# Kernel optimization log

Hardware: AMD Instinct MI355X
Metric: run time of the kernel (lower is better)

Reference implementation:

```python
import jax, jax.numpy as jnp
import numpy as np

N, E, R = 50000, 1600000, 8
IN_F, HID_F, OUT_F = 128, 64, 64


def setup_inputs() -> dict:
    key = jax.random.key(0)
    ks = jax.random.split(key, 9)
    x = jax.random.normal(ks[0], (N, IN_F), dtype=jnp.float32)
    edge_index = jax.random.randint(ks[1], (2, E), 0, N, dtype=jnp.int64)
    edge_type = jax.random.randint(ks[2], (E,), 0, R, dtype=jnp.int64)
    # layer 1 params (scaled like glorot)
    s1 = 1.0 / np.sqrt(IN_F)
    W1_rel = jax.random.normal(ks[3], (R, IN_F, HID_F), dtype=jnp.float32) * s1
    W1_root = jax.random.normal(ks[4], (IN_F, HID_F), dtype=jnp.float32) * s1
    b1 = jnp.zeros((HID_F,), dtype=jnp.float32)
    # layer 2 params
    s2 = 1.0 / np.sqrt(HID_F)
    W2_rel = jax.random.normal(ks[5], (R, HID_F, OUT_F), dtype=jnp.float32) * s2
    W2_root = jax.random.normal(ks[6], (HID_F, OUT_F), dtype=jnp.float32) * s2
    b2 = jnp.zeros((OUT_F,), dtype=jnp.float32)
    return {"x": x, "edge_index": edge_index, "edge_type": edge_type,
            "W1_rel": W1_rel, "W1_root": W1_root, "b1": b1,
            "W2_rel": W2_rel, "W2_root": W2_root, "b2": b2}


def _rgcn_conv(x, src, dst, etype, W_rel, W_root, b):
    """PyG RGCNConv: root transform + per-relation mean-aggregated messages."""
    n = x.shape[0]
    r = W_rel.shape[0]
    # per-relation transform of all node features: [R, N, H]
    xw = jnp.einsum('nd,rdh->rnh', x, W_rel)
    # per-edge message: transformed source feature under the edge's relation
    msg = xw[etype, src]  # [E, H]
    # mean normalization per (dst, relation) pair
    key = dst * r + etype  # [E]
    cnt = jax.ops.segment_sum(jnp.ones(etype.shape, dtype=x.dtype), key,
                              num_segments=n * r)
    inv = 1.0 / jnp.maximum(cnt, 1.0)
    msg = msg * inv[key][:, None]
    # scatter-add into target nodes
    agg = jax.ops.segment_sum(msg, dst, num_segments=n)  # [N, H]
    return agg + x @ W_root + b


def reference(x, edge_index, edge_type, W1_rel, W1_root, b1, W2_rel, W2_root, b2):
    src, dst = edge_index[0], edge_index[1]
    h = _rgcn_conv(x, src, dst, edge_type, W1_rel, W1_root, b1)
    h = jax.nn.relu(h)
    out = _rgcn_conv(h, src, dst, edge_type, W2_rel, W2_root, b2)
    return out
```

## Files before the change

kernel.cpp:

```cpp
#include <hip/hip_runtime.h>


constexpr int NN  = 50000;
constexpr int NE  = 1600000;
constexpr int NR  = 8;
constexpr int FIN = 128;
constexpr int FH  = 64;

constexpr int BSH = 7;
constexpr int BN  = 1 << BSH;
constexpr int NB  = (NN + BN - 1) >> BSH;
constexpr int CAP = 6144;
constexpr int CH  = 4096;
constexpr int NAPP = (NE + CH - 1) / CH;
constexpr unsigned XWMAX = (unsigned)(NN - 1) * (NR * 64) + (NR - 1) * 64;

typedef __attribute__((ext_vector_type(8))) short bf16x8;
typedef __attribute__((ext_vector_type(4))) short bf16x4;
typedef __attribute__((ext_vector_type(4))) float f32x4;

__device__ __forceinline__ unsigned short f2bf(float f) {
  unsigned u = __float_as_uint(f);
  u = (u + 0x7fff + ((u >> 16) & 1)) >> 16;
  return (unsigned short)u;
}
__device__ __forceinline__ float bf2f(unsigned short b) {
  return __uint_as_float(((unsigned)b) << 16);
}
__device__ __forceinline__ bool edge_ok(unsigned s, unsigned d, unsigned r) {
  return s < NN && d < NN && r < NR;
}

__global__ void __launch_bounds__(256) bucket_append(
    const int* __restrict__ src, const int* __restrict__ dst,
    const int* __restrict__ et, int* __restrict__ bcur,
    unsigned* __restrict__ brecs) {
  __shared__ uint2 stage[CH];
  __shared__ int h[NB], gbase[NB], sbase[NB], scur[NB];
  __shared__ int wtot[4];
  const int t  = threadIdx.x;
  const int c0 = blockIdx.x * CH;
  const int m  = min(CH, NE - c0);

  for (int i = t; i < NB; i += 256) h[i] = 0;
  __syncthreads();

  for (int i = t; i < m; i += 256) {
    const unsigned s = (unsigned)src[c0 + i];
    const unsigned d = (unsigned)dst[c0 + i];
    const unsigned r = (unsigned)et[c0 + i];
    if (edge_ok(s, d, r)) atomicAdd(&h[d >> BSH], 1);
  }
  __syncthreads();

  const int v0 = (2 * t < NB) ? h[2 * t] : 0;
  const int v1 = (2 * t + 1 < NB) ? h[2 * t + 1] : 0;
  if (2 * t < NB     && v0) gbase[2 * t]     = atomicAdd(&bcur[2 * t], v0);
  if (2 * t + 1 < NB && v1) gbase[2 * t + 1] = atomicAdd(&bcur[2 * t + 1], v1);
  const int s = v0 + v1;
  int incl = s;
#pragma unroll
  for (int o = 1; o < 64; o <<= 1) {
    int u = __shfl_up(incl, o, 64);
    if ((t & 63) >= o) incl += u;
  }
  if ((t & 63) == 63) wtot[t >> 6] = incl;
  __syncthreads();
  int wo = 0;
  for (int w = 0; w < (t >> 6); ++w) wo += wtot[w];
  const int e = wo + incl - s;
  if (2 * t < NB)     { sbase[2 * t] = e;          scur[2 * t] = e; }
  if (2 * t + 1 < NB) { sbase[2 * t + 1] = e + v0; scur[2 * t + 1] = e + v0; }
  __syncthreads();

  for (int i = t; i < m; i += 256) {
    const unsigned sv = (unsigned)src[c0 + i];
    const unsigned d  = (unsigned)dst[c0 + i];
    const unsigned r  = (unsigned)et[c0 + i];
    if (edge_ok(sv, d, r)) {
      const int p = atomicAdd(&scur[d >> BSH], 1);
      if (p < CH) stage[p] = make_uint2((sv << 10) | (((unsigned)d & (BN - 1)) << 3) | r, d);
    }
  }
  __syncthreads();

  const int M = min(sbase[NB - 1] + h[NB - 1], CH);
  for (int j = t; j < M; j += 256) {
    const uint2 rec = stage[j];
    const int b = (int)(rec.y >> BSH);
    const int idx = min(gbase[b] + (j - sbase[b]), NB * CAP - 1);
    brecs[idx] = rec.x;
  }
}

__global__ void __launch_bounds__(256) bucket_finalize(
    const int* __restrict__ bcur, const unsigned* __restrict__ brecs,
    int* __restrict__ row_start, int* __restrict__ deg,
    unsigned* __restrict__ recs) {
  const int b    = blockIdx.x;
  const int base = b * CAP;
  const int m    = min(bcur[b] - base, CAP);
  const int d0   = b << BSH;
  __shared__ int cnt[BN * NR];
  __shared__ int curs[BN * NR];
  __shared__ int wtot[4];
  const int t = threadIdx.x;

  for (int i = t; i < BN * NR; i += 256) cnt[i] = 0;
  __syncthreads();
  for (int i = t; i < m; i += 256) {
    const unsigned rec = brecs[base + i];
    const int dl = (int)((rec >> 3) & (BN - 1));
    const int r  = (int)(rec & 7);
    atomicAdd(&cnt[dl * NR + r], 1);
  }
  __syncthreads();

  const int c0 = cnt[t * 4], c1 = cnt[t * 4 + 1], c2 = cnt[t * 4 + 2], c3 = cnt[t * 4 + 3];
  const int s = c0 + c1 + c2 + c3;
  int incl = s;
#pragma unroll
  for (int o = 1; o < 64; o <<= 1) {
    int u = __shfl_up(incl, o, 64);
    if ((t & 63) >= o) incl += u;
  }
  if ((t & 63) == 63) wtot[t >> 6] = incl;
  __syncthreads();
  int wo = 0;
  for (int w = 0; w < (t >> 6); ++w) wo += wtot[w];
  const int e = wo + incl - s;
  curs[t * 4]     = e;
  curs[t * 4 + 1] = e + c0;
  curs[t * 4 + 2] = e + c0 + c1;
  curs[t * 4 + 3] = e + c0 + c1 + c2;
  __syncthreads();

  if (t < BN) {
    const int d = d0 + t;
    if (d < NN) {
      const int start = curs[t * NR];
      const int end   = (t == BN - 1) ? m : curs[(t + 1) * NR];
      row_start[d] = base + start;
      deg[d]       = end - start;
    }
  }
  __syncthreads();

  for (int i = t; i < m; i += 256) {
    const unsigned rec = brecs[base + i];
    const int dl = (int)((rec >> 3) & (BN - 1));
    const int r  = (int)(rec & 7);
    const unsigned sv = rec >> 10;
    const int p  = atomicAdd(&curs[dl * NR + r], 1);
    const unsigned cn = (unsigned)min(cnt[dl * NR + r], 127);
    recs[base + min(p, CAP - 1)] = (cn << 25) | (sv << 9) | ((unsigned)r << 6);
  }
}

__global__ void prep(const float* __restrict__ W1r, const float* __restrict__ W1o,
                     const float* __restrict__ W2r, const float* __restrict__ W2o,
                     unsigned short* __restrict__ Wt1,
                     unsigned short* __restrict__ Wt2,
                     int* __restrict__ bcur) {
  const int i  = blockIdx.x * blockDim.x + threadIdx.x;
  if (i < NB) bcur[i] = i * CAP;
  const int n1 = (NR + 1) * 64 * FIN;
  const int n2 = (NR + 1) * 64 * FH;
  if (i < n1) {
    const int g = i / (64 * FIN), rem = i % (64 * FIN);
    const int n = rem / FIN, k = rem % FIN;
    const float* W = (g < NR) ? (W1r + (size_t)g * FIN * 64) : W1o;
    Wt1[i] = f2bf(W[k * 64 + n]);
  } else if (i < n1 + n2) {
    const int j = i - n1;
    const int g = j / (64 * FH), rem = j % (64 * FH);
    const int n = rem / FH, k = rem % FH;
    const float* W = (g < NR) ? (W2r + (size_t)g * FH * 64) : W2o;
    Wt2[j] = f2bf(W[k * 64 + n]);
  }
}

template <int K, bool A_FP32, bool ROOT_BF16>
__device__ void gemm_body(char* smem, int bx,
                          const void* __restrict__ Av,
                          const unsigned short* __restrict__ Wt,
                          const float* __restrict__ bias,
                          unsigned short* __restrict__ xw,
                          void* __restrict__ root_out) {
  constexpr int KP  = K + 8;
  constexpr int NCH = 64 * (K / 8) / 256;
  constexpr int NKC = K / 32;
  unsigned short* Bs0 = (unsigned short*)smem;
  const int n0  = bx * 64;
  const int tid = threadIdx.x;
  const int wave = tid >> 6, lane = tid & 63;
  const int i16 = lane & 15, quad = lane >> 4;
  const int node = n0 + wave * 16 + i16;

  bf16x8 afrag[NKC];
  if constexpr (A_FP32) {
    const float* A = (const float*)Av;
#pragma unroll
    for (int kc = 0; kc < NKC; ++kc) {
      bf16x8 v = {};
      if (node < NN) {
        const float* p = A + (size_t)node * K + kc * 32 + quad * 8;
        const float4 f0 = *(const float4*)p;
        const float4 f1 = *(const float4*)(p + 4);
        v[0] = f2bf(f0.x); v[1] = f2bf(f0.y); v[2] = f2bf(f0.z); v[3] = f2bf(f0.w);
        v[4] = f2bf(f1.x); v[5] = f2bf(f1.y); v[6] = f2bf(f1.z); v[7] = f2bf(f1.w);
      }
      afrag[kc] = v;
    }
  } else {
    const unsigned short* A = (const unsigned short*)Av;
#pragma unroll
    for (int kc = 0; kc < NKC; ++kc) {
      bf16x8 v = {};
      if (node < NN) v = *(const bf16x8*)(A + (size_t)node * K + kc * 32 + quad * 8);
      afrag[kc] = v;
    }
  }

  for (int c = 0; c < NCH; ++c) {
    const int idx = tid + c * 256;
    const int row = idx / (K / 8), kp = (idx % (K / 8)) * 8;
    *(bf16x8*)(Bs0 + row * KP + kp) = *(const bf16x8*)(Wt + idx * 8);
  }
  __syncthreads();

  for (int g = 0; g <= NR; ++g) {
    const int buf = g & 1;
    unsigned short* Bc = Bs0 + buf * 64 * KP;
    unsigned short* Bn = Bs0 + (buf ^ 1) * 64 * KP;
    bf16x8 breg[NCH];
    if (g < NR) {
      const unsigned short* Wn = Wt + (size_t)(g + 1) * 64 * K;
#pragma unroll
      for (int c = 0; c < NCH; ++c) breg[c] = *(const bf16x8*)(Wn + (tid + c * 256) * 8);
    }

    f32x4 acc[4] = {};
#pragma unroll
    for (int kc = 0; kc < NKC; ++kc) {
      const int k0 = kc * 32 + quad * 8;
      const bf16x8 a0 = afrag[kc];
      const bf16x8 b0 = *(const bf16x8*)(Bc + (i16)      * KP + k0);
      const bf16x8 b1 = *(const bf16x8*)(Bc + (i16 + 16) * KP + k0);
      const bf16x8 b2 = *(const bf16x8*)(Bc + (i16 + 32) * KP + k0);
      const bf16x8 b3 = *(const bf16x8*)(Bc + (i16 + 48) * KP + k0);
      acc[0] = __builtin_amdgcn_mfma_f32_16x16x32_bf16(b0, a0, acc[0], 0, 0, 0);
      acc[1] = __builtin_amdgcn_mfma_f32_16x16x32_bf16(b1, a0, acc[1], 0, 0, 0);
      acc[2] = __builtin_amdgcn_mfma_f32_16x16x32_bf16(b2, a0, acc[2], 0, 0, 0);
      acc[3] = __builtin_amdgcn_mfma_f32_16x16x32_bf16(b3, a0, acc[3], 0, 0, 0);
    }

    if (g < NR) {
#pragma unroll
      for (int c = 0; c < NCH; ++c) {
        const int idx = tid + c * 256;
        const int row = idx / (K / 8), kp = (idx % (K / 8)) * 8;
        *(bf16x8*)(Bn + row * KP + kp) = breg[c];
      }
      if (node < NN) {
        unsigned short* p = xw + (size_t)node * (NR * 64) + g * 64 + quad * 4;
#pragma unroll
        for (int ct = 0; ct < 4; ++ct) {
          bf16x4 ov;
          ov[0] = (short)f2bf(acc[ct][0]); ov[1] = (short)f2bf(acc[ct][1]);
          ov[2] = (short)f2bf(acc[ct][2]); ov[3] = (short)f2bf(acc[ct][3]);
          *(bf16x4*)(p + ct * 16) = ov;
        }
      }
    } else if (node < NN) {
#pragma unroll
      for (int ct = 0; ct < 4; ++ct) {
        const float4 bv = *(const float4*)(bias + ct * 16 + quad * 4);
        const float o0 = acc[ct][0] + bv.x, o1 = acc[ct][1] + bv.y;
        const float o2 = acc[ct][2] + bv.z, o3 = acc[ct][3] + bv.w;
        if constexpr (ROOT_BF16) {
          unsigned short* p = (unsigned short*)root_out + (size_t)node * 64 + ct * 16 + quad * 4;
          bf16x4 ov;
          ov[0] = (short)f2bf(o0); ov[1] = (short)f2bf(o1);
          ov[2] = (short)f2bf(o2); ov[3] = (short)f2bf(o3);
          *(bf16x4*)p = ov;
        } else {
          float* p = (float*)root_out + (size_t)node * 64 + ct * 16 + quad * 4;
          *(float4*)p = make_float4(o0, o1, o2, o3);
        }
      }
    }
    __syncthreads();
  }
}

__global__ void __launch_bounds__(256) gemm_l1(
    const float* __restrict__ A, const unsigned short* __restrict__ Wt,
    const float* __restrict__ bias, unsigned short* __restrict__ xw,
    unsigned short* __restrict__ hroot) {
  extern __shared__ char smem[];
  gemm_body<FIN, true, true>(smem, (int)blockIdx.x, A, Wt, bias, xw, hroot);
}

__global__ void __launch_bounds__(256) gemm_l2(
    const unsigned short* __restrict__ A, const unsigned short* __restrict__ Wt,
    const float* __restrict__ bias, unsigned short* __restrict__ xw,
    float* __restrict__ out) {
  extern __shared__ char smem[];
  gemm_body<FH, false, false>(smem, (int)blockIdx.x, A, Wt, bias, xw, out);
}

template <bool RELU_BF16>
__global__ void __launch_bounds__(256) agg_csr(
    const int* __restrict__ row_start, const int* __restrict__ deg,
    const unsigned* __restrict__ recs, const unsigned short* __restrict__ xw,
    const void* __restrict__ rootv,
    float* __restrict__ out_f32, unsigned short* __restrict__ out_b16) {
  const int gid  = blockIdx.x * blockDim.x + threadIdx.x;
  const int lane = gid & 63;
  const int d    = gid >> 6;
  if (d >= NN) return;
  const int e  = lane >> 3;
  const int l8 = lane & 7;
  const int base = row_start[d];
  const int n    = deg[d];
  const unsigned* po = recs + base;
  const unsigned short* xp = xw + l8 * 8;
  float a[8] = {};

  int i0 = 0;
  for (; i0 + 32 < n; i0 += 64) {
    unsigned rr[8];
#pragma unroll
    for (int sl = 0; sl < 8; ++sl) {
      const int i = i0 + e + 8 * sl;
      rr[sl] = (i < n) ? po[i] : 0u;
    }
    bf16x8 vv[8];
#pragma unroll
    for (int sl = 0; sl < 4; ++sl) {
      const unsigned u = min(rr[sl] & 0x01FFFFFFu, XWMAX);
      vv[sl] = *(const bf16x8*)(xp + u);
    }
#pragma unroll
    for (int sl = 4; sl < 8; ++sl) {
      bf16x8 v = {};
      if (i0 + e + 8 * sl < n) {
        const unsigned u = min(rr[sl] & 0x01FFFFFFu, XWMAX);
        v = *(const bf16x8*)(xp + u);
      }
      vv[sl] = v;
    }
#pragma unroll
    for (int sl = 0; sl < 8; ++sl) {
      float w = __builtin_amdgcn_rcpf((float)(rr[sl] >> 25));
      if (i0 + e + 8 * sl >= n) w = 0.f;
#pragma unroll
      for (int q = 0; q < 8; ++q) a[q] += bf2f((unsigned short)vv[sl][q]) * w;
    }
  }
  if (i0 < n) {
    unsigned rr[4];
    bf16x8 vv[4];
#pragma unroll
    for (int sl = 0; sl < 4; ++sl) {
      const int i = i0 + e + 8 * sl;
      rr[sl] = (i < n) ? po[i] : 0u;
    }
#pragma unroll
    for (int sl = 0; sl < 4; ++sl) {
      bf16x8 v = {};
      if (i0 + e + 8 * sl < n) {
        const unsigned u = min(rr[sl] & 0x01FFFFFFu, XWMAX);
        v = *(const bf16x8*)(xp + u);
      }
      vv[sl] = v;
    }
#pragma unroll
    for (int sl = 0; sl < 4; ++sl) {
      float w = __builtin_amdgcn_rcpf((float)(rr[sl] >> 25));
      if (i0 + e + 8 * sl >= n) w = 0.f;
#pragma unroll
      for (int q = 0; q < 8; ++q) a[q] += bf2f((unsigned short)vv[sl][q]) * w;
    }
  }

#pragma unroll
  for (int q = 0; q < 8; ++q) {
    a[q] += __shfl_xor(a[q], 8, 64);
    a[q] += __shfl_xor(a[q], 16, 64);
    a[q] += __shfl_xor(a[q], 32, 64);
  }

  if (e == 0) {
    float r[8];
    if constexpr (RELU_BF16) {
      const bf16x8 rv = *(const bf16x8*)((const unsigned short*)rootv + (size_t)d * 64 + l8 * 8);
#pragma unroll
      for (int q = 0; q < 8; ++q) r[q] = bf2f((unsigned short)rv[q]);
    } else {
      const float4 r0 = *(const float4*)((const float*)rootv + (size_t)d * 64 + l8 * 8);
      const float4 r1 = *(const float4*)((const float*)rootv + (size_t)d * 64 + l8 * 8 + 4);
      r[0] = r0.x; r[1] = r0.y; r[2] = r0.z; r[3] = r0.w;
      r[4] = r1.x; r[5] = r1.y; r[6] = r1.z; r[7] = r1.w;
    }
    float o[8];
#pragma unroll
    for (int q = 0; q < 8; ++q) o[q] = r[q] + a[q];
    if (RELU_BF16) {
      bf16x8 ov;
#pragma unroll
      for (int q = 0; q < 8; ++q) ov[q] = (short)f2bf(fmaxf(o[q], 0.f));
      *(bf16x8*)(out_b16 + (size_t)d * 64 + l8 * 8) = ov;
    } else {
      *(float4*)(out_f32 + (size_t)d * 64 + l8 * 8)     = make_float4(o[0], o[1], o[2], o[3]);
      *(float4*)(out_f32 + (size_t)d * 64 + l8 * 8 + 4) = make_float4(o[4], o[5], o[6], o[7]);
    }
  }
}

extern "C" void kernel_launch(void* const* d_in, const int* in_sizes, int n_in,
                              void* d_out, int out_size, void* d_ws, size_t ws_size,
                              hipStream_t stream) {
  const float* x   = (const float*)d_in[0];
  const int*   ei  = (const int*)d_in[1];
  const int*   et  = (const int*)d_in[2];
  const float* W1r = (const float*)d_in[3];
  const float* W1o = (const float*)d_in[4];
  const float* b1  = (const float*)d_in[5];
  const float* W2r = (const float*)d_in[6];
  const float* W2o = (const float*)d_in[7];
  const float* b2  = (const float*)d_in[8];
  float* out = (float*)d_out;

  const int* src = ei;
  const int* dst = ei + NE;

  char* ws = (char*)d_ws;
  size_t off = 0;
  auto alloc = [&](size_t bytes) {
    void* p = ws + off; off += (bytes + 255) & ~(size_t)255; return p;
  };
  int*   bcur      = (int*)alloc((size_t)NB * 4);
  int*   row_start = (int*)alloc((size_t)NN * 4);
  int*   deg       = (int*)alloc((size_t)NN * 4);
  unsigned* brecs  = (unsigned*)alloc((size_t)NB * CAP * 4);
  unsigned* offs   = (unsigned*)alloc((size_t)NB * CAP * 4);
  unsigned short* xw    = (unsigned short*)alloc((size_t)NN * NR * 64 * 2);
  unsigned short* hb    = (unsigned short*)alloc((size_t)NN * FH * 2);
  unsigned short* hroot = (unsigned short*)alloc((size_t)NN * 64 * 2);
  unsigned short* Wt1   = (unsigned short*)alloc((size_t)(NR + 1) * 64 * FIN * 2);
  unsigned short* Wt2   = (unsigned short*)alloc((size_t)(NR + 1) * 64 * FH * 2);

  const int nprep = (NR + 1) * 64 * (FIN + FH);
  prep<<<(nprep + 255) / 256, 256, 0, stream>>>(W1r, W1o, W2r, W2o, Wt1, Wt2, bcur);

  const int gemm_blocks = (NN + 63) / 64;
  const int agg_blocks  = (NN * 64 + 255) / 256;
  constexpr int SM1 = 2 * 64 * (FIN + 8) * 2;
  constexpr int SM2 = 2 * 64 * (FH + 8) * 2;

  bucket_append<<<NAPP, 256, 0, stream>>>(src, dst, et, bcur, brecs);
  bucket_finalize<<<NB, 256, 0, stream>>>(bcur, brecs, row_start, deg, offs);

  gemm_l1<<<gemm_blocks, 256, SM1, stream>>>(x, Wt1, b1, xw, hroot);
  agg_csr<true><<<agg_blocks, 256, 0, stream>>>(row_start, deg, offs, xw, hroot, nullptr, hb);
  gemm_l2<<<gemm_blocks, 256, SM2, stream>>>(hb, Wt2, b2, xw, out);
  agg_csr<false><<<agg_blocks, 256, 0, stream>>>(row_start, deg, offs, xw, out, out, nullptr);
}
```

Measured before the change: 265.3 us.

## Fuse edge bucketing with layer-1 GEMM and layer-1 aggregation with layer-2 GEMM

Merges the edge bucket-append kernel into the layer-1 GEMM launch by interleaving append blocks among GEMM blocks, so the two independent stages share one grid. It also fuses layer-1 aggregation with the layer-2 transform: each block aggregates 64 nodes into a shared-memory tile and runs the MFMA GEMM on it directly, avoiding the global round trip through the hidden activations and two launches. The trade-off is that the fused agg+GEMM kernel uses one wave per 16 nodes processed serially, which lowers memory-level parallelism for the gather. It also needs separate xw buffers and an extra fp32 root buffer.

Result: faster. 253.8 us (-4.3%).

```diff
diff --git a/kernel.cpp b/kernel.cpp
--- a/kernel.cpp
+++ b/kernel.cpp
@@ -31,15 +31,21 @@
   return s < NN && d < NN && r < NR;
 }
 
-__global__ void __launch_bounds__(256) bucket_append(
-    const int* __restrict__ src, const int* __restrict__ dst,
-    const int* __restrict__ et, int* __restrict__ bcur,
-    unsigned* __restrict__ brecs) {
-  __shared__ uint2 stage[CH];
-  __shared__ int h[NB], gbase[NB], sbase[NB], scur[NB];
-  __shared__ int wtot[4];
+__device__ void append_body(char* smem, int bx,
+                            const int* __restrict__ src,
+                            const int* __restrict__ dst,
+                            const int* __restrict__ et,
+                            int* __restrict__ bcur,
+                            unsigned* __restrict__ brecs) {
+  uint2* stage = (uint2*)smem;
+  int* h     = (int*)(smem + (size_t)CH * 8);
+  int* gbase = h + NB;
+  int* sbase = gbase + NB;
+  int* scur  = sbase + NB;
+  int* wtot  = scur + NB;
+
   const int t  = threadIdx.x;
-  const int c0 = blockIdx.x * CH;
+  const int c0 = bx * CH;
   const int m  = min(CH, NE - c0);
 
   for (int i = t; i < NB; i += 256) h[i] = 0;
@@ -294,28 +300,160 @@
   }
 }
 
-__global__ void __launch_bounds__(256) gemm_l1(
+__global__ void __launch_bounds__(256) fused_append_gemm1(
+    const int* __restrict__ src, const int* __restrict__ dst,
+    const int* __restrict__ et, int* __restrict__ bcur,
+    unsigned* __restrict__ brecs,
     const float* __restrict__ A, const unsigned short* __restrict__ Wt,
     const float* __restrict__ bias, unsigned short* __restrict__ xw,
     unsigned short* __restrict__ hroot) {
   extern __shared__ char smem[];
-  gemm_body<FIN, true, true>(smem, (int)blockIdx.x, A, Wt, bias, xw, hroot);
-}
-
-__global__ void __launch_bounds__(256) gemm_l2(
-    const unsigned short* __restrict__ A, const unsigned short* __restrict__ Wt,
-    const float* __restrict__ bias, unsigned short* __restrict__ xw,
-    float* __restrict__ out) {
-  extern __shared__ char smem[];
-  gemm_body<FH, false, false>(smem, (int)blockIdx.x, A, Wt, bias, xw, out);
-}
-
-template <bool RELU_BF16>
-__global__ void __launch_bounds__(256) agg_csr(
+  const int bx = (int)blockIdx.x;
+  if (bx % 3 == 2 && bx / 3 < NAPP)
+    append_body(smem, bx / 3, src, dst, et, bcur, brecs);
+  else
+    gemm_body<FIN, true, true>(smem, bx - (bx + 1) / 3, A, Wt, bias, xw, hroot);
+}
+
+constexpr int KP2 = 80;
+
+__global__ void __launch_bounds__(256) agg1_gemm2(
     const int* __restrict__ row_start, const int* __restrict__ deg,
     const unsigned* __restrict__ recs, const unsigned short* __restrict__ xw,
-    const void* __restrict__ rootv,
-    float* __restrict__ out_f32, unsigned short* __restrict__ out_b16) {
+    const unsigned short* __restrict__ hroot,
+    const unsigned short* __restrict__ Wt2, const float* __restrict__ b2,
+    unsigned short* __restrict__ xw2, float* __restrict__ root2) {
+  __shared__ unsigned short hb_s[64 * KP2];
+  __shared__ unsigned short Bs0[2 * 64 * KP2];
+  const int tid = threadIdx.x;
+  const int wave = tid >> 6, lane = tid & 63;
+  const int e = lane >> 3, l8 = lane & 7;
+  const int n0 = (int)blockIdx.x * 64;
+
+  for (int j = 0; j < 16; ++j) {
+    const int row = wave * 16 + j;
+    const int d = n0 + row;
+    float a[8] = {};
+    if (d < NN) {
+      const int base = row_start[d];
+      const int n    = deg[d];
+      const unsigned* po = recs + base;
+      const unsigned short* xp = xw + l8 * 8;
+      for (int i0 = 0; i0 < n; i0 += 32) {
+        unsigned rr[4];
+#pragma unroll
+        for (int sl = 0; sl < 4; ++sl) {
+          const int i = i0 + e + 8 * sl;
+          rr[sl] = (i < n) ? po[i] : 0u;
+        }
+        bf16x8 vv[4];
+#pragma unroll
+        for (int sl = 0; sl < 4; ++sl) {
+          const unsigned u = min(rr[sl] & 0x01FFFFFFu, XWMAX);
+          vv[sl] = *(const bf16x8*)(xp + u);
+        }
+#pragma unroll
+        for (int sl = 0; sl < 4; ++sl) {
+          float w = __builtin_amdgcn_rcpf((float)(rr[sl] >> 25));
+          if (i0 + e + 8 * sl >= n) w = 0.f;
+#pragma unroll
+          for (int q = 0; q < 8; ++q) a[q] += bf2f((unsigned short)vv[sl][q]) * w;
+        }
+      }
+    }
+#pragma unroll
+    for (int q = 0; q < 8; ++q) {
+      a[q] += __shfl_xor(a[q], 8, 64);
+      a[q] += __shfl_xor(a[q], 16, 64);
+      a[q] += __shfl_xor(a[q], 32, 64);
+    }
+    if (e == 0) {
+      bf16x8 hv = {};
+      if (d < NN) {
+        const bf16x8 rv = *(const bf16x8*)(hroot + (size_t)d * 64 + l8 * 8);
+#pragma unroll
+        for (int q = 0; q < 8; ++q)
+          hv[q] = (short)f2bf(fmaxf(bf2f((unsigned short)rv[q]) + a[q], 0.f));
+      }
+      *(bf16x8*)(hb_s + row * KP2 + l8 * 8) = hv;
+    }
+  }
+
+#pragma unroll
+  for (int c = 0; c < 2; ++c) {
+    const int idx = tid + c * 256;
+    const int rown = idx >> 3, kp = (idx & 7) * 8;
+    *(bf16x8*)(Bs0 + rown * KP2 + kp) = *(const bf16x8*)(Wt2 + idx * 8);
+  }
+  __syncthreads();
+
+  const int i16 = lane & 15, quad = lane >> 4;
+  const int node = n0 + wave * 16 + i16;
+  bf16x8 afrag[2];
+#pragma unroll
+  for (int kc = 0; kc < 2; ++kc)
+    afrag[kc] = *(const bf16x8*)(hb_s + (wave * 16 + i16) * KP2 + kc * 32 + quad * 8);
+
+  for (int g = 0; g <= NR; ++g) {
+    const int buf = g & 1;
+    unsigned short* Bc = Bs0 + buf * 64 * KP2;
+    unsigned short* Bn = Bs0 + (buf ^ 1) * 64 * KP2;
+    bf16x8 breg[2];
+    if (g < NR) {
+      const unsigned short* Wn = Wt2 + (size_t)(g + 1) * 64 * FH;
+#pragma unroll
+      for (int c = 0; c < 2; ++c) breg[c] = *(const bf16x8*)(Wn + (tid + c * 256) * 8);
+    }
+
+    f32x4 acc[4] = {};
+#pragma unroll
+    for (int kc = 0; kc < 2; ++kc) {
+      const int k0 = kc * 32 + quad * 8;
+      const bf16x8 a0 = afrag[kc];
+      const bf16x8 b0 = *(const bf16x8*)(Bc + (i16)      * KP2 + k0);
+      const bf16x8 b1 = *(const bf16x8*)(Bc + (i16 + 16) * KP2 + k0);
+      const bf16x8 b2v = *(const bf16x8*)(Bc + (i16 + 32) * KP2 + k0);
+      const bf16x8 b3 = *(const bf16x8*)(Bc + (i16 + 48) * KP2 + k0);
+      acc[0] = __builtin_amdgcn_mfma_f32_16x16x32_bf16(b0,  a0, acc[0], 0, 0, 0);
+      acc[1] = __builtin_amdgcn_mfma_f32_16x16x32_bf16(b1,  a0, acc[1], 0, 0, 0);
+      acc[2] = __builtin_amdgcn_mfma_f32_16x16x32_bf16(b2v, a0, acc[2], 0, 0, 0);
+      acc[3] = __builtin_amdgcn_mfma_f32_16x16x32_bf16(b3,  a0, acc[3], 0, 0, 0);
+    }
+
+    if (g < NR) {
+#pragma unroll
+      for (int c = 0; c < 2; ++c) {
+        const int idx = tid + c * 256;
+        const int rown = idx >> 3, kp = (idx & 7) * 8;
+        *(bf16x8*)(Bn + rown * KP2 + kp) = breg[c];
+      }
+      if (node < NN) {
+        unsigned short* p = xw2 + (size_t)node * (NR * 64) + g * 64 + quad * 4;
+#pragma unroll
+        for (int ct = 0; ct < 4; ++ct) {
+          bf16x4 ov;
+          ov[0] = (short)f2bf(acc[ct][0]); ov[1] = (short)f2bf(acc[ct][1]);
+          ov[2] = (short)f2bf(acc[ct][2]); ov[3] = (short)f2bf(acc[ct][3]);
+          *(bf16x4*)(p + ct * 16) = ov;
+        }
+      }
+    } else if (node < NN) {
+#pragma unroll
+      for (int ct = 0; ct < 4; ++ct) {
+        const float4 bv = *(const float4*)(b2 + ct * 16 + quad * 4);
+        float* p = root2 + (size_t)node * 64 + ct * 16 + quad * 4;
+        *(float4*)p = make_float4(acc[ct][0] + bv.x, acc[ct][1] + bv.y,
+                                  acc[ct][2] + bv.z, acc[ct][3] + bv.w);
+      }
+    }
+    __syncthreads();
+  }
+}
+
+__global__ void __launch_bounds__(256) agg2(
+    const int* __restrict__ row_start, const int* __restrict__ deg,
+    const unsigned* __restrict__ recs, const unsigned short* __restrict__ xw,
+    const float* __restrict__ root, float* __restrict__ out_f32) {
   const int gid  = blockIdx.x * blockDim.x + threadIdx.x;
   const int lane = gid & 63;
   const int d    = gid >> 6;
@@ -338,43 +476,30 @@
     }
     bf16x8 vv[8];
 #pragma unroll
+    for (int sl = 0; sl < 8; ++sl) {
+      const unsigned u = min(rr[sl] & 0x01FFFFFFu, XWMAX);
+      vv[sl] = *(const bf16x8*)(xp + u);
+    }
+#pragma unroll
+    for (int sl = 0; sl < 8; ++sl) {
+      float w = __builtin_amdgcn_rcpf((float)(rr[sl] >> 25));
+      if (i0 + e + 8 * sl >= n) w = 0.f;
+#pragma unroll
+      for (int q = 0; q < 8; ++q) a[q] += bf2f((unsigned short)vv[sl][q]) * w;
+    }
+  }
+  if (i0 < n) {
+    unsigned rr[4];
+#pragma unroll
+    for (int sl = 0; sl < 4; ++sl) {
+      const int i = i0 + e + 8 * sl;
+      rr[sl] = (i < n) ? po[i] : 0u;
+    }
+    bf16x8 vv[4];
+#pragma unroll
     for (int sl = 0; sl < 4; ++sl) {
       const unsigned u = min(rr[sl] & 0x01FFFFFFu, XWMAX);
       vv[sl] = *(const bf16x8*)(xp + u);
-    }
-#pragma unroll
-    for (int sl = 4; sl < 8; ++sl) {
-      bf16x8 v = {};
-      if (i0 + e + 8 * sl < n) {
-        const unsigned u = min(rr[sl] & 0x01FFFFFFu, XWMAX);
-        v = *(const bf16x8*)(xp + u);
-      }
-      vv[sl] = v;
-    }
-#pragma unroll
-    for (int sl = 0; sl < 8; ++sl) {
-      float w = __builtin_amdgcn_rcpf((float)(rr[sl] >> 25));
-      if (i0 + e + 8 * sl >= n) w = 0.f;
-#pragma unroll
-      for (int q = 0; q < 8; ++q) a[q] += bf2f((unsigned short)vv[sl][q]) * w;
-    }
-  }
-  if (i0 < n) {
-    unsigned rr[4];
-    bf16x8 vv[4];
-#pragma unroll
-    for (int sl = 0; sl < 4; ++sl) {
-      const int i = i0 + e + 8 * sl;
-      rr[sl] = (i < n) ? po[i] : 0u;
-    }
-#pragma unroll
-    for (int sl = 0; sl < 4; ++sl) {
-      bf16x8 v = {};
-      if (i0 + e + 8 * sl < n) {
-        const unsigned u = min(rr[sl] & 0x01FFFFFFu, XWMAX);
-        v = *(const bf16x8*)(xp + u);
-      }
-      vv[sl] = v;
     }
 #pragma unroll
     for (int sl = 0; sl < 4; ++sl) {
@@ -393,29 +518,12 @@
   }
 
   if (e == 0) {
-    float r[8];
-    if constexpr (RELU_BF16) {
-      const bf16x8 rv = *(const bf16x8*)((const unsigned short*)rootv + (size_t)d * 64 + l8 * 8);
-#pragma unroll
-      for (int q = 0; q < 8; ++q) r[q] = bf2f((unsigned short)rv[q]);
-    } else {
-      const float4 r0 = *(const float4*)((const float*)rootv + (size_t)d * 64 + l8 * 8);
-      const float4 r1 = *(const float4*)((const float*)rootv + (size_t)d * 64 + l8 * 8 + 4);
-      r[0] = r0.x; r[1] = r0.y; r[2] = r0.z; r[3] = r0.w;
-      r[4] = r1.x; r[5] = r1.y; r[6] = r1.z; r[7] = r1.w;
-    }
-    float o[8];
-#pragma unroll
-    for (int q = 0; q < 8; ++q) o[q] = r[q] + a[q];
-    if (RELU_BF16) {
-      bf16x8 ov;
-#pragma unroll
-      for (int q = 0; q < 8; ++q) ov[q] = (short)f2bf(fmaxf(o[q], 0.f));
-      *(bf16x8*)(out_b16 + (size_t)d * 64 + l8 * 8) = ov;
-    } else {
-      *(float4*)(out_f32 + (size_t)d * 64 + l8 * 8)     = make_float4(o[0], o[1], o[2], o[3]);
-      *(float4*)(out_f32 + (size_t)d * 64 + l8 * 8 + 4) = make_float4(o[4], o[5], o[6], o[7]);
-    }
+    const float4 r0 = *(const float4*)(root + (size_t)d * 64 + l8 * 8);
+    const float4 r1 = *(const float4*)(root + (size_t)d * 64 + l8 * 8 + 4);
+    *(float4*)(out_f32 + (size_t)d * 64 + l8 * 8) =
+        make_float4(r0.x + a[0], r0.y + a[1], r0.z + a[2], r0.w + a[3]);
+    *(float4*)(out_f32 + (size_t)d * 64 + l8 * 8 + 4) =
+        make_float4(r1.x + a[4], r1.y + a[5], r1.z + a[6], r1.w + a[7]);
   }
 }
 
@@ -446,9 +554,10 @@
   int*   deg       = (int*)alloc((size_t)NN * 4);
   unsigned* brecs  = (unsigned*)alloc((size_t)NB * CAP * 4);
   unsigned* offs   = (unsigned*)alloc((size_t)NB * CAP * 4);
-  unsigned short* xw    = (unsigned short*)alloc((size_t)NN * NR * 64 * 2);
-  unsigned short* hb    = (unsigned short*)alloc((size_t)NN * FH * 2);
+  unsigned short* xw1   = (unsigned short*)alloc((size_t)NN * NR * 64 * 2);
+  unsigned short* xw2   = (unsigned short*)alloc((size_t)NN * NR * 64 * 2);
   unsigned short* hroot = (unsigned short*)alloc((size_t)NN * 64 * 2);
+  float*          root2 = (float*)alloc((size_t)NN * 64 * 4);
   unsigned short* Wt1   = (unsigned short*)alloc((size_t)(NR + 1) * 64 * FIN * 2);
   unsigned short* Wt2   = (unsigned short*)alloc((size_t)(NR + 1) * 64 * FH * 2);
 
@@ -456,15 +565,15 @@
   prep<<<(nprep + 255) / 256, 256, 0, stream>>>(W1r, W1o, W2r, W2o, Wt1, Wt2, bcur);
 
   const int gemm_blocks = (NN + 63) / 64;
-  const int agg_blocks  = (NN * 64 + 255) / 256;
-  constexpr int SM1 = 2 * 64 * (FIN + 8) * 2;
-  constexpr int SM2 = 2 * 64 * (FH + 8) * 2;
-
-  bucket_append<<<NAPP, 256, 0, stream>>>(src, dst, et, bcur, brecs);
+  const int agg2_blocks = (NN * 64 + 255) / 256;
+  const int ag_blocks   = (NN + 63) / 64;
+  constexpr int SM1 = CH * 8 + 4 * NB * 4 + 16;
+
+  fused_append_gemm1<<<NAPP + gemm_blocks, 256, SM1, stream>>>(
+      src, dst, et, bcur, brecs, x, Wt1, b1, xw1, hroot);
   bucket_finalize<<<NB, 256, 0, stream>>>(bcur, brecs, row_start, deg, offs);
 
-  gemm_l1<<<gemm_blocks, 256, SM1, stream>>>(x, Wt1, b1, xw, hroot);
-  agg_csr<true><<<agg_blocks, 256, 0, stream>>>(row_start, deg, offs, xw, hroot, nullptr, hb);
-  gemm_l2<<<gemm_blocks, 256, SM2, stream>>>(hb, Wt2, b2, xw, out);
-  agg_csr<false><<<agg_blocks, 256, 0, stream>>>(row_start, deg, offs, xw, out, out, nullptr);
-}
+  agg1_gemm2<<<ag_blocks, 256, 0, stream>>>(row_start, deg, offs, xw1, hroot,
+                                            Wt2, b2, xw2, root2);
+  agg2<<<agg2_blocks, 256, 0, stream>>>(row_start, deg, offs, xw2, root2, out);
+}
```

## Fuse edge bucketing into layer-1 GEMM launch and make xw relation-major

Applied to the files above, without the earlier changes.

Edge-bucket append blocks now run inside the layer-1 GEMM kernel, interleaved one append block per two GEMM blocks, so edge bucketing overlaps with the dense transform instead of running as its own launch. The per-relation transformed features are stored relation-major ([R][N][64]). Edge records now encode the (relation, source) row offset directly. The aggregation loads drop the bounds clamp and predication, relying on padded records pointing at row 0. Layer 2's root output goes to a separate buffer rather than aliasing the output. This raises shared memory per block for the fused kernel and mixes two very different block workloads in one grid.

Result: faster. 245.3 us (-7.5%).

```diff
diff --git a/kernel.cpp b/kernel.cpp
--- a/kernel.cpp
+++ b/kernel.cpp
@@ -13,7 +13,6 @@
 constexpr int CAP = 6144;
 constexpr int CH  = 4096;
 constexpr int NAPP = (NE + CH - 1) / CH;
-constexpr unsigned XWMAX = (unsigned)(NN - 1) * (NR * 64) + (NR - 1) * 64;
 
 typedef __attribute__((ext_vector_type(8))) short bf16x8;
 typedef __attribute__((ext_vector_type(4))) short bf16x4;
@@ -31,15 +30,21 @@
   return s < NN && d < NN && r < NR;
 }
 
-__global__ void __launch_bounds__(256) bucket_append(
-    const int* __restrict__ src, const int* __restrict__ dst,
-    const int* __restrict__ et, int* __restrict__ bcur,
-    unsigned* __restrict__ brecs) {
-  __shared__ uint2 stage[CH];
-  __shared__ int h[NB], gbase[NB], sbase[NB], scur[NB];
-  __shared__ int wtot[4];
+__device__ void append_body(char* smem, int bx,
+                            const int* __restrict__ src,
+                            const int* __restrict__ dst,
+                            const int* __restrict__ et,
+                            int* __restrict__ bcur,
+                            unsigned* __restrict__ brecs) {
+  uint2* stage = (uint2*)smem;
+  int* h     = (int*)(smem + (size_t)CH * 8);
+  int* gbase = h + NB;
+  int* sbase = gbase + NB;
+  int* scur  = sbase + NB;
+  int* wtot  = scur + NB;
+
   const int t  = threadIdx.x;
-  const int c0 = blockIdx.x * CH;
+  const int c0 = bx * CH;
   const int m  = min(CH, NE - c0);
 
   for (int i = t; i < NB; i += 256) h[i] = 0;
@@ -153,7 +158,7 @@
     const unsigned sv = rec >> 10;
     const int p  = atomicAdd(&curs[dl * NR + r], 1);
     const unsigned cn = (unsigned)min(cnt[dl * NR + r], 127);
-    recs[base + min(p, CAP - 1)] = (cn << 25) | (sv << 9) | ((unsigned)r << 6);
+    recs[base + min(p, CAP - 1)] = (cn << 25) | (((unsigned)r * NN + sv) << 6);
   }
 }
 
@@ -263,7 +268,7 @@
         *(bf16x8*)(Bn + row * KP + kp) = breg[c];
       }
       if (node < NN) {
-        unsigned short* p = xw + (size_t)node * (NR * 64) + g * 64 + quad * 4;
+        unsigned short* p = xw + (size_t)g * (NN * 64) + (size_t)node * 64 + quad * 4;
 #pragma unroll
         for (int ct = 0; ct < 4; ++ct) {
           bf16x4 ov;
@@ -294,12 +299,19 @@
   }
 }
 
-__global__ void __launch_bounds__(256) gemm_l1(
+__global__ void __launch_bounds__(256) fused_append_gemm1(
+    const int* __restrict__ src, const int* __restrict__ dst,
+    const int* __restrict__ et, int* __restrict__ bcur,
+    unsigned* __restrict__ brecs,
     const float* __restrict__ A, const unsigned short* __restrict__ Wt,
     const float* __restrict__ bias, unsigned short* __restrict__ xw,
     unsigned short* __restrict__ hroot) {
   extern __shared__ char smem[];
-  gemm_body<FIN, true, true>(smem, (int)blockIdx.x, A, Wt, bias, xw, hroot);
+  const int bx = (int)blockIdx.x;
+  if (bx % 3 == 2 && bx / 3 < NAPP)
+    append_body(smem, bx / 3, src, dst, et, bcur, brecs);
+  else
+    gemm_body<FIN, true, true>(smem, bx - (bx + 1) / 3, A, Wt, bias, xw, hroot);
 }
 
 __global__ void __launch_bounds__(256) gemm_l2(
@@ -338,19 +350,8 @@
     }
     bf16x8 vv[8];
 #pragma unroll
-    for (int sl = 0; sl < 4; ++sl) {
-      const unsigned u = min(rr[sl] & 0x01FFFFFFu, XWMAX);
-      vv[sl] = *(const bf16x8*)(xp + u);
-    }
-#pragma unroll
-    for (int sl = 4; sl < 8; ++sl) {
-      bf16x8 v = {};
-      if (i0 + e + 8 * sl < n) {
-        const unsigned u = min(rr[sl] & 0x01FFFFFFu, XWMAX);
-        v = *(const bf16x8*)(xp + u);
-      }
-      vv[sl] = v;
-    }
+    for (int sl = 0; sl < 8; ++sl)
+      vv[sl] = *(const bf16x8*)(xp + (rr[sl] & 0x01FFFFFFu));
 #pragma unroll
     for (int sl = 0; sl < 8; ++sl) {
       float w = __builtin_amdgcn_rcpf((float)(rr[sl] >> 25));
@@ -361,21 +362,15 @@
   }
   if (i0 < n) {
     unsigned rr[4];
-    bf16x8 vv[4];
 #pragma unroll
     for (int sl = 0; sl < 4; ++sl) {
       const int i = i0 + e + 8 * sl;
       rr[sl] = (i < n) ? po[i] : 0u;
     }
-#pragma unroll
-    for (int sl = 0; sl < 4; ++sl) {
-      bf16x8 v = {};
-      if (i0 + e + 8 * sl < n) {
-        const unsigned u = min(rr[sl] & 0x01FFFFFFu, XWMAX);
-        v = *(const bf16x8*)(xp + u);
-      }
-      vv[sl] = v;
-    }
+    bf16x8 vv[4];
+#pragma unroll
+    for (int sl = 0; sl < 4; ++sl)
+      vv[sl] = *(const bf16x8*)(xp + (rr[sl] & 0x01FFFFFFu));
 #pragma unroll
     for (int sl = 0; sl < 4; ++sl) {
       float w = __builtin_amdgcn_rcpf((float)(rr[sl] >> 25));
@@ -449,6 +444,7 @@
   unsigned short* xw    = (unsigned short*)alloc((size_t)NN * NR * 64 * 2);
   unsigned short* hb    = (unsigned short*)alloc((size_t)NN * FH * 2);
   unsigned short* hroot = (unsigned short*)alloc((size_t)NN * 64 * 2);
+  float*          root2 = (float*)alloc((size_t)NN * 64 * 4);
   unsigned short* Wt1   = (unsigned short*)alloc((size_t)(NR + 1) * 64 * FIN * 2);
   unsigned short* Wt2   = (unsigned short*)alloc((size_t)(NR + 1) * 64 * FH * 2);
 
@@ -457,14 +453,14 @@
 
   const int gemm_blocks = (NN + 63) / 64;
   const int agg_blocks  = (NN * 64 + 255) / 256;
-  constexpr int SM1 = 2 * 64 * (FIN + 8) * 2;
+  constexpr int SM1 = CH * 8 + 4 * NB * 4 + 16;
   constexpr int SM2 = 2 * 64 * (FH + 8) * 2;
 
-  bucket_append<<<NAPP, 256, 0, stream>>>(src, dst, et, bcur, brecs);
+  fused_append_gemm1<<<NAPP + gemm_blocks, 256, SM1, stream>>>(
+      src, dst, et, bcur, brecs, x, Wt1, b1, xw, hroot);
   bucket_finalize<<<NB, 256, 0, stream>>>(bcur, brecs, row_start, deg, offs);
 
-  gemm_l1<<<gemm_blocks, 256, SM1, stream>>>(x, Wt1, b1, xw, hroot);
   agg_csr<true><<<agg_blocks, 256, 0, stream>>>(row_start, deg, offs, xw, hroot, nullptr, hb);
-  gemm_l2<<<gemm_blocks, 256, SM2, stream>>>(hb, Wt2, b2, xw, out);
-  agg_csr<false><<<agg_blocks, 256, 0, stream>>>(row_start, deg, offs, xw, out, out, nullptr);
-}
+  gemm_l2<<<gemm_blocks, 256, SM2, stream>>>(hb, Wt2, b2, xw, root2);
+  agg_csr<false><<<agg_blocks, 256, 0, stream>>>(row_start, deg, offs, xw, root2, out, nullptr);
+}
```
